# Performance work log

Hardware: AMD Instinct MI355X
Metric: run time of the kernel (lower is better)

The kernel has to match this reference:

```python
import jax, jax.numpy as jnp
import numpy as np


def setup_inputs() -> dict:
    key = jax.random.key(0)
    k1, k2, k3, k4 = jax.random.split(key, 4)
    B, S, D = 8, 2048, 512
    scale = 1.0 / np.sqrt(D)
    return {
        "x": jax.random.normal(k1, (B, S, D), dtype=jnp.float32),
        "WQ": jax.random.normal(k2, (D, D), dtype=jnp.float32) * scale,
        "WK": jax.random.normal(k3, (D, D), dtype=jnp.float32) * scale,
        "WV": jax.random.normal(k4, (D, D), dtype=jnp.float32) * scale,
    }


def reference(x, WQ, WK, WV):
    # x: [B, S, D]; single-head scaled dot-product self-attention
    Q = jnp.einsum("bsd,de->bse", x, WQ)
    K = jnp.einsum("bsd,de->bse", x, WK)
    V = jnp.einsum("bsd,de->bse", x, WV)
    d_k = jnp.asarray(K.shape[-1], dtype=x.dtype)
    scores = jnp.einsum("bqd,bkd->bqk", Q, K) / jnp.sqrt(d_k)  # [B,S,S]
    weights = jax.nn.softmax(scores, axis=-1)
    return jnp.einsum("bqk,bkd->bqd", weights, V)
```

## Files before the change

### kernel.cpp

```cpp
#include <hip/hip_runtime.h>
#include <cstdint>
#include <cstddef>

#define B_ 8
#define S_ 2048
#define D_ 512

typedef float f32x4 __attribute__((ext_vector_type(4)));
typedef __bf16 bf16x8 __attribute__((ext_vector_type(8)));

__device__ __forceinline__ unsigned short f2bf(float f) {
    unsigned u = __builtin_bit_cast(unsigned, f);
    u += 0x7FFFu + ((u >> 16) & 1u);
    return (unsigned short)(u >> 16);
}

__device__ __forceinline__ void gll16(const void* g, void* l) {
    __builtin_amdgcn_global_load_lds(
        (const __attribute__((address_space(1))) unsigned int*)g,
        (__attribute__((address_space(3))) unsigned int*)l, 16, 0, 0);
}

#define VMCNT(n) asm volatile("s_waitcnt vmcnt(%0)" :: "i"(n) : "memory")
#define SBAR()   __builtin_amdgcn_s_barrier()
#define SCHED0() __builtin_amdgcn_sched_barrier(0)

template<int AMT, int BNT>
__global__ __launch_bounds__(512, 2) void gemm8(
    const unsigned short* __restrict__ A,
    const unsigned short* __restrict__ B,
    void* __restrict__ Cv,
    unsigned short* __restrict__ Cv2,
    float* __restrict__ rs_part,
    int K, int lda, int ldb, int ldc,
    long long sA, long long sB, long long sC,
    float scale, int mode, int ntn, int nbatch)
{
    constexpr int BM     = 64 * AMT;
    constexpr int BN     = 128 * BNT;
    constexpr int ABYTES = BM * 128;
    constexpr int BBYTES = BN * 128;
    constexpr int AH     = ABYTES / 2;
    constexpr int BH     = BBYTES / 2;
    constexpr int AGL    = AMT / 2;
    constexpr int BGL    = BNT;
    constexpr int BUFB   = ABYTES + BBYTES;
    __shared__ __align__(16) char lds[2 * BUFB];

    const int lin = blockIdx.x;
    const int bz  = lin % nbatch;
    const int tq  = lin / nbatch;
    const int tn  = tq % ntn;
    const int tm  = tq / ntn;
    A += (long long)bz * sA;
    B += (long long)bz * sB;
    const int m0   = tm * BM;
    const int n0   = tn * BN;
    const int tid  = threadIdx.x;
    const int lane = tid & 63;
    const int w    = tid >> 6;
    const int g2   = w >> 2;
    const int nb   = w & 3;

    const int lrow = lane >> 3;
    const int swz  = ((lane & 7) ^ lrow) << 3;
    const unsigned short* gA[2][AGL];
    const unsigned short* gB[2][BGL];
    #pragma unroll
    for (int h = 0; h < 2; ++h) {
        #pragma unroll
        for (int i = 0; i < AGL; ++i)
            gA[h][i] = A + (size_t)(m0 + h * (BM / 2) + (w * AGL + i) * 8 + lrow) * lda + swz;
        #pragma unroll
        for (int i = 0; i < BGL; ++i)
            gB[h][i] = B + (size_t)(n0 + h * (BN / 2) + (w * BGL + i) * 8 + lrow) * ldb + swz;
    }
    auto stA = [&](int bs, int h, int kof) {
        #pragma unroll
        for (int i = 0; i < AGL; ++i)
            gll16(gA[h][i] + kof, lds + bs * BUFB + h * AH + (w * AGL + i) * 1024);
    };
    auto stB = [&](int bs, int h, int kof) {
        #pragma unroll
        for (int i = 0; i < BGL; ++i)
            gll16(gB[h][i] + kof, lds + bs * BUFB + ABYTES + h * BH + (w * BGL + i) * 1024);
    };

    const int fr = lane & 15;
    const int gq = lane >> 4;
    const int c0 = (gq ^ (fr & 7)) << 4;
    int aoff[AMT], boff[BNT];
    #pragma unroll
    for (int ml = 0; ml < AMT; ++ml)
        aoff[ml] = (g2 * (16 * AMT) + ml * 16 + fr) * 128 + c0;
    #pragma unroll
    for (int nl = 0; nl < BNT; ++nl)
        boff[nl] = (nb * (16 * BNT) + nl * 16 + fr) * 128 + c0;

    bf16x8 af[2 * AMT], bLO[2 * BNT], bHI[2 * BNT];
    f32x4 acc[2 * AMT][2 * BNT] = {};

    auto ldA = [&](const char* Ab, int mh) {
        #pragma unroll
        for (int ml = 0; ml < AMT; ++ml)
            #pragma unroll
            for (int kk = 0; kk < 2; ++kk)
                af[ml * 2 + kk] = *(const bf16x8*)(Ab + mh * AH + (aoff[ml] ^ (kk << 6)));
    };
    auto ldB = [&](const char* Bb, int nh, bf16x8* bf) {
        #pragma unroll
        for (int nl = 0; nl < BNT; ++nl)
            #pragma unroll
            for (int kk = 0; kk < 2; ++kk)
                bf[nl * 2 + kk] = *(const bf16x8*)(Bb + nh * BH + (boff[nl] ^ (kk << 6)));
    };
    auto mma = [&](int mh, int nh, const bf16x8* bf) {
        __builtin_amdgcn_s_setprio(1);
        #pragma unroll
        for (int ml = 0; ml < AMT; ++ml)
            #pragma unroll
            for (int nl = 0; nl < BNT; ++nl)
                #pragma unroll
                for (int kk = 0; kk < 2; ++kk)
                    acc[mh * AMT + ml][nh * BNT + nl] =
                        __builtin_amdgcn_mfma_f32_16x16x32_bf16(
                            af[ml * 2 + kk], bf[nl * 2 + kk],
                            acc[mh * AMT + ml][nh * BNT + nl], 0, 0, 0);
        __builtin_amdgcn_s_setprio(0);
    };

    stA(0, 0, 0); stB(0, 0, 0); stB(0, 1, 0); stA(0, 1, 0);
    VMCNT(AGL + BGL);
    SBAR();
    SCHED0();

    const int NT = K >> 6;
    for (int tt = 0; tt < NT; ++tt) {
        const int bs = tt & 1;
        const char* Ab = lds + bs * BUFB;
        const char* Bb = Ab + ABYTES;
        const int  nk  = (tt + 1) << 6;
        const bool pf  = (tt + 1 < NT);

        ldA(Ab, 0); ldB(Bb, 0, bLO);
        if (pf) stA(bs ^ 1, 0, nk);
        SCHED0();
        if (pf) { VMCNT(2 * AGL); } else { VMCNT(AGL); }
        SBAR();
        SCHED0();
        mma(0, 0, bLO);
        SBAR();
        SCHED0();

        ldB(Bb, 1, bHI);
        if (pf) stB(bs ^ 1, 0, nk);
        SCHED0();
        if (pf) { VMCNT(AGL + BGL); } else { VMCNT(0); }
        SBAR();
        SCHED0();
        mma(0, 1, bHI);
        SBAR();
        SCHED0();

        ldA(Ab, 1);
        if (pf) stB(bs ^ 1, 1, nk);
        SCHED0();
        SBAR();
        SCHED0();
        mma(1, 0, bLO);
        SBAR();
        SCHED0();

        if (pf) { stA(bs ^ 1, 1, nk); SCHED0(); VMCNT(AGL + BGL); }
        SBAR();
        SCHED0();
        mma(1, 1, bHI);
        SBAR();
        SCHED0();
    }

    const int rb4 = gq << 2;
#define AB_(mt) ((((mt) / AMT) * (BM / 2)) + g2 * (16 * AMT) + ((mt) % AMT) * 16)
#define BB_(nt) ((((nt) / BNT) * (BN / 2)) + nb * (16 * BNT) + ((nt) % BNT) * 16)

    if (mode == 1) {
        #pragma unroll
        for (int mt = 0; mt < 2 * AMT; ++mt)
            #pragma unroll
            for (int nt = 0; nt < 2 * BNT; ++nt)
                #pragma unroll
                for (int r = 0; r < 4; ++r)
                    acc[mt][nt][r] = __expf(acc[mt][nt][r] * scale);

        unsigned short* C = (unsigned short*)Cv + (long long)bz * sC;
        #pragma unroll
        for (int mt = 0; mt < 2 * AMT; ++mt)
            #pragma unroll
            for (int nt = 0; nt < 2 * BNT; ++nt) {
                const int gc = n0 + BB_(nt) + fr;
                #pragma unroll
                for (int r = 0; r < 4; ++r)
                    C[(size_t)(m0 + AB_(mt) + rb4 + r) * ldc + gc] = f2bf(acc[mt][nt][r]);
            }

        float* rp = rs_part + (((long long)bz * S_) << 5) + tn * 4 + nb;
        #pragma unroll
        for (int mt = 0; mt < 2 * AMT; ++mt)
            #pragma unroll
            for (int r = 0; r < 4; ++r) {
                float s = 0.f;
                #pragma unroll
                for (int nt = 0; nt < 2 * BNT; ++nt) s += acc[mt][nt][r];
                s += __shfl_xor(s, 8);
                s += __shfl_xor(s, 4);
                s += __shfl_xor(s, 2);
                s += __shfl_xor(s, 1);
                if (fr == 0)
                    rp[(long long)(m0 + AB_(mt) + rb4 + r) << 5] = s;
            }
    } else if (mode == 3) {
        if (tn >= 4) {
            #pragma unroll
            for (int mt = 0; mt < 2 * AMT; ++mt) {
                const int s0q = m0 + AB_(mt) + rb4;
                const int b   = s0q >> 11;
                const int se  = s0q & (S_ - 1);
                #pragma unroll
                for (int nt = 0; nt < 2 * BNT; ++nt) {
                    const int d = (n0 - 2 * D_) + BB_(nt) + fr;
                    ushort4 u;
                    u.x = f2bf(acc[mt][nt][0]);
                    u.y = f2bf(acc[mt][nt][1]);
                    u.z = f2bf(acc[mt][nt][2]);
                    u.w = f2bf(acc[mt][nt][3]);
                    *(ushort4*)&Cv2[((size_t)b * D_ + d) * S_ + se] = u;
                }
            }
        } else {
            unsigned short* C = (unsigned short*)Cv;
            #pragma unroll
            for (int mt = 0; mt < 2 * AMT; ++mt)
                #pragma unroll
                for (int nt = 0; nt < 2 * BNT; ++nt) {
                    const int gc = n0 + BB_(nt) + fr;
                    #pragma unroll
                    for (int r = 0; r < 4; ++r)
                        C[(size_t)(m0 + AB_(mt) + rb4 + r) * ldc + gc] = f2bf(acc[mt][nt][r]);
                }
        }
    } else {
        float* C = (float*)Cv + (long long)bz * sC;
        #pragma unroll
        for (int nt = 0; nt < 2 * BNT; ++nt) {
            const int q = n0 + BB_(nt) + fr;
            const float* rp = rs_part + (((long long)bz * S_ + q) << 5);
            float ssum = 0.f;
            #pragma unroll
            for (int pq = 0; pq < 8; ++pq) {
                const float4 p4 = *(const float4*)(rp + 4 * pq);
                ssum += (p4.x + p4.y) + (p4.z + p4.w);
            }
            const float inv = __builtin_amdgcn_rcpf(ssum);
            #pragma unroll
            for (int mt = 0; mt < 2 * AMT; ++mt) {
                const int d0 = m0 + AB_(mt) + rb4;
                float4 o;
                o.x = acc[mt][nt][0] * inv;
                o.y = acc[mt][nt][1] * inv;
                o.z = acc[mt][nt][2] * inv;
                o.w = acc[mt][nt][3] * inv;
                *(float4*)&C[(size_t)q * ldc + d0] = o;
            }
        }
    }
#undef AB_
#undef BB_
}

__global__ __launch_bounds__(256) void convert_x4(const float* __restrict__ x,
                                                  unsigned short* __restrict__ xb) {
    const size_t i = ((size_t)blockIdx.x * 256 + threadIdx.x) * 4;
    const float4 f = *(const float4*)(x + i);
    ushort4 u;
    u.x = f2bf(f.x); u.y = f2bf(f.y); u.z = f2bf(f.z); u.w = f2bf(f.w);
    *(ushort4*)(xb + i) = u;
}

__global__ __launch_bounds__(256) void convert_w(const float* __restrict__ WQ,
                                                 const float* __restrict__ WK,
                                                 const float* __restrict__ WV,
                                                 unsigned short* __restrict__ WT) {
    const int o = blockIdx.x * 256 + threadIdx.x;
    const float* W = blockIdx.y == 0 ? WQ : (blockIdx.y == 1 ? WK : WV);
    const int e = o >> 9, d = o & (D_ - 1);
    WT[(size_t)blockIdx.y * D_ * D_ + o] = f2bf(W[d * D_ + e]);
}

extern "C" void kernel_launch(void* const* d_in, const int* in_sizes, int n_in,
                              void* d_out, int out_size, void* d_ws, size_t ws_size,
                              hipStream_t stream)
{
    const float* x  = (const float*)d_in[0];
    const float* WQ = (const float*)d_in[1];
    const float* WK = (const float*)d_in[2];
    const float* WV = (const float*)d_in[3];

    unsigned short* ws  = (unsigned short*)d_ws;
    const size_t NX = (size_t)B_ * S_ * D_;
    unsigned short* xb  = ws;
    unsigned short* wtb = xb + NX;
    unsigned short* qk  = wtb + 3 * D_ * D_;
    unsigned short* vtb = qk + NX * 2;
    unsigned short* sb  = vtb + NX;
    float* rsp = (float*)(sb + (size_t)B_ * S_ * S_);

    convert_x4<<<dim3((unsigned)(NX / 4 / 256)), 256, 0, stream>>>(x, xb);
    convert_w<<<dim3(D_ * D_ / 256, 3), 256, 0, stream>>>(WQ, WK, WV, wtb);

    gemm8<4, 2><<<dim3(384), 512, 0, stream>>>(
        xb, wtb, qk, vtb, nullptr, D_, D_, D_, 2 * D_,
        0, 0, 0, 1.0f, 3,  6,  1);

    gemm8<4, 2><<<dim3(512), 512, 0, stream>>>(
        qk , qk + D_ , sb, nullptr, rsp, D_, 2 * D_, 2 * D_, S_,
        (long long)S_ * 2 * D_, (long long)S_ * 2 * D_, (long long)S_ * S_,
        0.04419417382415922f, 1,  8,  8);

    gemm8<2, 2><<<dim3(256), 512, 0, stream>>>(
        vtb, sb, d_out, nullptr, rsp, S_, S_, S_, D_,
        (long long)D_ * S_, (long long)S_ * S_, (long long)S_ * D_,
        1.0f, 0,  8,  8);
}
```

Baseline: 232.9 us.

## Software-pipeline LDS fragment loads one stage ahead of the MFMA blocks

Splits the A-fragment LDS reads into halves and preloads the next tile's first A half and B half before the last MFMA block of the current tile. Each MFMA block then overlaps with the LDS reads for the block after it, and the vmcnt waits are relaxed to match the new order. The aim is to hide LDS read latency behind matrix math. The cost is extra register pressure from the afp buffer and the fragment copies, which may lower occupancy or cause spills.

```diff
diff --git a/kernel.cpp b/kernel.cpp
--- a/kernel.cpp
+++ b/kernel.cpp
@@ -97,15 +97,16 @@
     for (int nl = 0; nl < BNT; ++nl)
         boff[nl] = (nb * (16 * BNT) + nl * 16 + fr) * 128 + c0;
 
-    bf16x8 af[2 * AMT], bLO[2 * BNT], bHI[2 * BNT];
+    bf16x8 af[2 * AMT], afp[AMT], bLO[2 * BNT], bHI[2 * BNT];
     f32x4 acc[2 * AMT][2 * BNT] = {};
 
-    auto ldA = [&](const char* Ab, int mh) {
-        #pragma unroll
-        for (int ml = 0; ml < AMT; ++ml)
+    auto ldA_h = [&](const char* Ab, int mh, int hh, bf16x8* dst) {
+        #pragma unroll
+        for (int ml = 0; ml < AMT / 2; ++ml)
             #pragma unroll
             for (int kk = 0; kk < 2; ++kk)
-                af[ml * 2 + kk] = *(const bf16x8*)(Ab + mh * AH + (aoff[ml] ^ (kk << 6)));
+                dst[ml * 2 + kk] = *(const bf16x8*)(
+                    Ab + mh * AH + (aoff[hh * (AMT / 2) + ml] ^ (kk << 6)));
     };
     auto ldB = [&](const char* Bb, int nh, bf16x8* bf) {
         #pragma unroll
@@ -130,53 +131,54 @@
     };
 
     stA(0, 0, 0); stB(0, 0, 0); stB(0, 1, 0); stA(0, 1, 0);
-    VMCNT(AGL + BGL);
+    VMCNT(AGL);
     SBAR();
     SCHED0();
+    ldA_h(lds, 0, 0, afp);
+    ldB(lds + ABYTES, 0, bLO);
 
     const int NT = K >> 6;
     for (int tt = 0; tt < NT; ++tt) {
         const int bs = tt & 1;
-        const char* Ab = lds + bs * BUFB;
-        const char* Bb = Ab + ABYTES;
+        const char* Ab  = lds + bs * BUFB;
+        const char* Bb  = Ab + ABYTES;
+        const char* Abn = lds + (bs ^ 1) * BUFB;
+        const char* Bbn = Abn + ABYTES;
         const int  nk  = (tt + 1) << 6;
         const bool pf  = (tt + 1 < NT);
 
-        ldA(Ab, 0); ldB(Bb, 0, bLO);
+        #pragma unroll
+        for (int j = 0; j < AMT; ++j) af[j] = afp[j];
+        ldA_h(Ab, 0, 1, af + AMT);
+        ldB(Bb, 1, bHI);
         if (pf) stA(bs ^ 1, 0, nk);
         SCHED0();
-        if (pf) { VMCNT(2 * AGL); } else { VMCNT(AGL); }
-        SBAR();
-        SCHED0();
+        if (pf) { VMCNT(AGL); } else { VMCNT(0); }
+        SBAR(); SCHED0();
         mma(0, 0, bLO);
-        SBAR();
-        SCHED0();
-
-        ldB(Bb, 1, bHI);
+        SBAR(); SCHED0();
+
+        ldA_h(Ab, 1, 0, afp);
         if (pf) stB(bs ^ 1, 0, nk);
         SCHED0();
-        if (pf) { VMCNT(AGL + BGL); } else { VMCNT(0); }
-        SBAR();
-        SCHED0();
+        SBAR(); SCHED0();
         mma(0, 1, bHI);
-        SBAR();
-        SCHED0();
-
-        ldA(Ab, 1);
+        SBAR(); SCHED0();
+
+        #pragma unroll
+        for (int j = 0; j < AMT; ++j) af[j] = afp[j];
+        ldA_h(Ab, 1, 1, af + AMT);
         if (pf) stB(bs ^ 1, 1, nk);
         SCHED0();
-        SBAR();
-        SCHED0();
+        SBAR(); SCHED0();
         mma(1, 0, bLO);
-        SBAR();
-        SCHED0();
-
-        if (pf) { stA(bs ^ 1, 1, nk); SCHED0(); VMCNT(AGL + BGL); }
-        SBAR();
-        SCHED0();
+        SBAR(); SCHED0();
+
+        if (pf) { stA(bs ^ 1, 1, nk); SCHED0(); VMCNT(AGL); }
+        SBAR(); SCHED0();
+        if (pf) { ldA_h(Abn, 0, 0, afp); ldB(Bbn, 0, bLO); }
         mma(1, 1, bHI);
-        SBAR();
-        SCHED0();
+        SBAR(); SCHED0();
     }
 
     const int rb4 = gq << 2;
```

Result: slower. 239.5 us (+2.8%).
